# Performance work log

Measured on AMD Instinct MI355X. Metric: run time of the kernel, lower is better.

## Reference

```python
import jax, jax.numpy as jnp
import numpy as np

EM_STEPS = 2
C, N, H, F = 32, 200000, 4, 64


def setup_inputs() -> dict:
    key = jax.random.key(0)
    kq, kk, kv = jax.random.split(key, 3)
    Q = jax.random.normal(kq, (C, H, F), dtype=jnp.float32)
    K = jax.random.normal(kk, (N, H, F), dtype=jnp.float32)
    V = jax.random.normal(kv, (N, H, F), dtype=jnp.float32)
    return {"Q": Q, "K": K, "V": V}


def reference(Q, K, V):
    # EM-style recurrent cross-attention:
    #   scores[c,n,h] = sum_f centroid[c,h,f] * K[n,h,f] / sqrt(F)
    #   weights = softmax over clusters (axis 0)
    #   centroid[c,h,f] = sum_n weights[c,n,h] * V[n,h,f]
    scale = 1.0 / np.sqrt(np.float32(Q.shape[-1]))
    centroid = Q
    for _ in range(EM_STEPS):
        scores = jnp.einsum('chf,nhf->cnh', centroid, K) * scale  # (C,N,H)
        weights = jax.nn.softmax(scores, axis=0)                  # over clusters
        centroid = jnp.einsum('cnh,nhf->chf', weights, V)         # (C,H,F)
    return centroid
```

## Files before the change

### kernel.cpp

```cpp
#include <hip/hip_runtime.h>


#define CC 32
#define HH 4
#define FF 64
#define NB 64
#define WAVES 4
#define BLOCK 256
#define GX 192

__global__ __launch_bounds__(BLOCK, 3) void em_step_kernel(
    const float* __restrict__ cent_in,
    const float* __restrict__ Kp,
    const float* __restrict__ Vp,
    float* __restrict__ cent_out,
    int N)
{
    const int h    = blockIdx.y;
    const int tid  = threadIdx.x;
    const int wid  = tid >> 6;
    const int lane = tid & 63;

    __shared__ float cent[CC][FF];
    __shared__ float wlds[WAVES][NB][36];

    #pragma unroll
    for (int k = 0; k < (CC * FF) / BLOCK; ++k) {
        int i = k * BLOCK + tid;
        int c = i >> 6, f = i & 63;
        cent[c][f] = cent_in[(c * HH + h) * FF + f] * 0.125f;
    }
    __syncthreads();

    float acc[CC];
    #pragma unroll
    for (int c = 0; c < CC; ++c) acc[c] = 0.f;

    const int ngroups = (N + NB - 1) / NB;

    for (int g = blockIdx.x * WAVES + wid; g < ngroups; g += GX * WAVES) {
        const int n0 = g * NB;

        const int  n     = n0 + lane;
        const bool valid = (n < N);
        const int  ncl   = valid ? n : (N - 1);
        const float4* Kr = (const float4*)(Kp + ((size_t)ncl * HH + h) * FF);

        float s[CC];
        #pragma unroll
        for (int c = 0; c < CC; ++c) s[c] = 0.f;

        #pragma unroll 4
        for (int f4 = 0; f4 < FF / 4; ++f4) {
            float4 k4 = Kr[f4];
            #pragma unroll
            for (int c = 0; c < CC; ++c) {
                float4 ce = *(const float4*)&cent[c][f4 * 4];
                s[c] = fmaf(k4.x, ce.x, s[c]);
                s[c] = fmaf(k4.y, ce.y, s[c]);
                s[c] = fmaf(k4.z, ce.z, s[c]);
                s[c] = fmaf(k4.w, ce.w, s[c]);
            }
        }

        float m = s[0];
        #pragma unroll
        for (int c = 1; c < CC; ++c) m = fmaxf(m, s[c]);
        float sum = 0.f;
        #pragma unroll
        for (int c = 0; c < CC; ++c) { s[c] = __expf(s[c] - m); sum += s[c]; }
        float r = 1.0f / sum;
        if (!valid) r = 0.f;

        float4* wr = (float4*)&wlds[wid][lane][0];
        #pragma unroll
        for (int c4 = 0; c4 < 8; ++c4) {
            float4 w4;
            w4.x = s[c4 * 4 + 0] * r;
            w4.y = s[c4 * 4 + 1] * r;
            w4.z = s[c4 * 4 + 2] * r;
            w4.w = s[c4 * 4 + 3] * r;
            wr[c4] = w4;
        }

        #pragma unroll 4
        for (int j = 0; j < NB; ++j) {
            int nj  = n0 + j;
            int njc = nj < N ? nj : (N - 1);
            float v = Vp[((size_t)njc * HH + h) * FF + lane];
            #pragma unroll
            for (int c4 = 0; c4 < 8; ++c4) {
                float4 w4 = *(const float4*)&wlds[wid][j][c4 * 4];
                acc[c4 * 4 + 0] = fmaf(w4.x, v, acc[c4 * 4 + 0]);
                acc[c4 * 4 + 1] = fmaf(w4.y, v, acc[c4 * 4 + 1]);
                acc[c4 * 4 + 2] = fmaf(w4.z, v, acc[c4 * 4 + 2]);
                acc[c4 * 4 + 3] = fmaf(w4.w, v, acc[c4 * 4 + 3]);
            }
        }
    }

    __syncthreads();
    float* red = &wlds[0][0][0];
    #pragma unroll
    for (int c = 0; c < CC; ++c) red[(wid * CC + c) * FF + lane] = acc[c];
    __syncthreads();
    #pragma unroll
    for (int k = 0; k < (CC * FF) / BLOCK; ++k) {
        int o = k * BLOCK + tid;
        int c = o >> 6, f = o & 63;
        float val = red[(0 * CC + c) * FF + f]
                  + red[(1 * CC + c) * FF + f]
                  + red[(2 * CC + c) * FF + f]
                  + red[(3 * CC + c) * FF + f];
        atomicAdd(&cent_out[(c * HH + h) * FF + f], val);
    }
}

extern "C" void kernel_launch(void* const* d_in, const int* in_sizes, int n_in,
                              void* d_out, int out_size, void* d_ws, size_t ws_size,
                              hipStream_t stream)
{
    const float* Q = (const float*)d_in[0];
    const float* K = (const float*)d_in[1];
    const float* V = (const float*)d_in[2];
    float*       out   = (float*)d_out;
    float*       cent1 = (float*)d_ws;

    const int N = in_sizes[1] / (HH * FF);

    hipMemsetAsync(cent1, 0, CC * HH * FF * sizeof(float), stream);
    hipMemsetAsync(out,   0, CC * HH * FF * sizeof(float), stream);

    dim3 grid(GX, HH), block(BLOCK);
    em_step_kernel<<<grid, block, 0, stream>>>(Q,     K, V, cent1, N);
    em_step_kernel<<<grid, block, 0, stream>>>(cent1, K, V, out,   N);
}
```

Baseline: 894.7 us.

## Use packed FP32 FMA, transposed centroid LDS, and double-buffered V loads

Result: faster. 727.7 us (-18.7%).

```diff
diff --git a/kernel.cpp b/kernel.cpp
--- a/kernel.cpp
+++ b/kernel.cpp
@@ -5,11 +5,17 @@
 #define HH 4
 #define FF 64
 #define NB 64
-#define WAVES 4
-#define BLOCK 256
-#define GX 192
+#define WAVES 8
+#define BLOCK 512
+#define GX 128
 
-__global__ __launch_bounds__(BLOCK, 3) void em_step_kernel(
+typedef float f32x2 __attribute__((ext_vector_type(2)));
+
+__device__ __forceinline__ void pkfma(f32x2& d, f32x2 a, f32x2 b) {
+    asm("v_pk_fma_f32 %0, %1, %2, %0" : "+v"(d) : "v"(a), "v"(b));
+}
+
+__global__ __launch_bounds__(BLOCK, 4) void em_step_kernel(
     const float* __restrict__ cent_in,
     const float* __restrict__ Kp,
     const float* __restrict__ Vp,
@@ -21,20 +27,18 @@
     const int wid  = tid >> 6;
     const int lane = tid & 63;
 
-    __shared__ float cent[CC][FF];
+    __shared__ float centT[FF][CC];
     __shared__ float wlds[WAVES][NB][36];
 
-    #pragma unroll
-    for (int k = 0; k < (CC * FF) / BLOCK; ++k) {
-        int i = k * BLOCK + tid;
-        int c = i >> 6, f = i & 63;
-        cent[c][f] = cent_in[(c * HH + h) * FF + f] * 0.125f;
+    for (int i = tid; i < CC * FF; i += BLOCK) {
+        int c = i & (CC - 1), f = i >> 5;
+        centT[f][c] = cent_in[(c * HH + h) * FF + f] * 0.125f;
     }
     __syncthreads();
 
-    float acc[CC];
+    f32x2 acc2[16];
     #pragma unroll
-    for (int c = 0; c < CC; ++c) acc[c] = 0.f;
+    for (int p = 0; p < 16; ++p) acc2[p] = f32x2{0.f, 0.f};
 
     const int ngroups = (N + NB - 1) / NB;
 
@@ -46,29 +50,36 @@
         const int  ncl   = valid ? n : (N - 1);
         const float4* Kr = (const float4*)(Kp + ((size_t)ncl * HH + h) * FF);
 
-        float s[CC];
+        f32x2 s2[16];
         #pragma unroll
-        for (int c = 0; c < CC; ++c) s[c] = 0.f;
+        for (int p = 0; p < 16; ++p) s2[p] = f32x2{0.f, 0.f};
 
         #pragma unroll 4
         for (int f4 = 0; f4 < FF / 4; ++f4) {
             float4 k4 = Kr[f4];
+            float kv[4] = {k4.x, k4.y, k4.z, k4.w};
             #pragma unroll
-            for (int c = 0; c < CC; ++c) {
-                float4 ce = *(const float4*)&cent[c][f4 * 4];
-                s[c] = fmaf(k4.x, ce.x, s[c]);
-                s[c] = fmaf(k4.y, ce.y, s[c]);
-                s[c] = fmaf(k4.z, ce.z, s[c]);
-                s[c] = fmaf(k4.w, ce.w, s[c]);
+            for (int ff = 0; ff < 4; ++ff) {
+                f32x2 kk = {kv[ff], kv[ff]};
+                const float4* crow = (const float4*)&centT[f4 * 4 + ff][0];
+                #pragma unroll
+                for (int c8 = 0; c8 < 8; ++c8) {
+                    float4 ce = crow[c8];
+                    pkfma(s2[c8 * 2 + 0], kk, f32x2{ce.x, ce.y});
+                    pkfma(s2[c8 * 2 + 1], kk, f32x2{ce.z, ce.w});
+                }
             }
         }
 
-        float m = s[0];
+        float m = -3.0e38f;
         #pragma unroll
-        for (int c = 1; c < CC; ++c) m = fmaxf(m, s[c]);
+        for (int p = 0; p < 16; ++p) m = fmaxf(m, fmaxf(s2[p].x, s2[p].y));
         float sum = 0.f;
         #pragma unroll
-        for (int c = 0; c < CC; ++c) { s[c] = __expf(s[c] - m); sum += s[c]; }
+        for (int p = 0; p < 16; ++p) {
+            s2[p].x = __expf(s2[p].x - m); sum += s2[p].x;
+            s2[p].y = __expf(s2[p].y - m); sum += s2[p].y;
+        }
         float r = 1.0f / sum;
         if (!valid) r = 0.f;
 
@@ -76,42 +87,64 @@
         #pragma unroll
         for (int c4 = 0; c4 < 8; ++c4) {
             float4 w4;
-            w4.x = s[c4 * 4 + 0] * r;
-            w4.y = s[c4 * 4 + 1] * r;
-            w4.z = s[c4 * 4 + 2] * r;
-            w4.w = s[c4 * 4 + 3] * r;
+            w4.x = s2[2 * c4].x     * r;
+            w4.y = s2[2 * c4].y     * r;
+            w4.z = s2[2 * c4 + 1].x * r;
+            w4.w = s2[2 * c4 + 1].y * r;
             wr[c4] = w4;
         }
 
-        #pragma unroll 4
-        for (int j = 0; j < NB; ++j) {
-            int nj  = n0 + j;
-            int njc = nj < N ? nj : (N - 1);
-            float v = Vp[((size_t)njc * HH + h) * FF + lane];
+        const float* Vb = Vp + (size_t)h * FF + lane;
+
+        auto loadv = [&](float (&buf)[16], int jbase) {
             #pragma unroll
-            for (int c4 = 0; c4 < 8; ++c4) {
-                float4 w4 = *(const float4*)&wlds[wid][j][c4 * 4];
-                acc[c4 * 4 + 0] = fmaf(w4.x, v, acc[c4 * 4 + 0]);
-                acc[c4 * 4 + 1] = fmaf(w4.y, v, acc[c4 * 4 + 1]);
-                acc[c4 * 4 + 2] = fmaf(w4.z, v, acc[c4 * 4 + 2]);
-                acc[c4 * 4 + 3] = fmaf(w4.w, v, acc[c4 * 4 + 3]);
+            for (int jj = 0; jj < 16; ++jj) {
+                int nj  = n0 + jbase + jj;
+                int njc = nj < N ? nj : (N - 1);
+                buf[jj] = Vb[(size_t)njc * (HH * FF)];
             }
-        }
+        };
+        auto pv = [&](const float (&buf)[16], int jbase) {
+            #pragma unroll
+            for (int jj = 0; jj < 16; ++jj) {
+                int j = jbase + jj;
+                f32x2 vv = {buf[jj], buf[jj]};
+                const float4* wrow = (const float4*)&wlds[wid][j][0];
+                #pragma unroll
+                for (int c4 = 0; c4 < 8; ++c4) {
+                    float4 w4 = wrow[c4];
+                    pkfma(acc2[2 * c4 + 0], vv, f32x2{w4.x, w4.y});
+                    pkfma(acc2[2 * c4 + 1], vv, f32x2{w4.z, w4.w});
+                }
+            }
+        };
+
+        float va[16], vb[16];
+        loadv(va, 0);
+        loadv(vb, 16);
+        pv(va, 0);
+        loadv(va, 32);
+        pv(vb, 16);
+        loadv(vb, 48);
+        pv(va, 32);
+        pv(vb, 48);
     }
 
     __syncthreads();
     float* red = &wlds[0][0][0];
     #pragma unroll
-    for (int c = 0; c < CC; ++c) red[(wid * CC + c) * FF + lane] = acc[c];
+    for (int p = 0; p < 16; ++p) {
+        red[(wid * CC + 2 * p + 0) * FF + lane] = acc2[p].x;
+        red[(wid * CC + 2 * p + 1) * FF + lane] = acc2[p].y;
+    }
     __syncthreads();
     #pragma unroll
     for (int k = 0; k < (CC * FF) / BLOCK; ++k) {
         int o = k * BLOCK + tid;
         int c = o >> 6, f = o & 63;
-        float val = red[(0 * CC + c) * FF + f]
-                  + red[(1 * CC + c) * FF + f]
-                  + red[(2 * CC + c) * FF + f]
-                  + red[(3 * CC + c) * FF + f];
+        float val = 0.f;
+        #pragma unroll
+        for (int w = 0; w < WAVES; ++w) val += red[(w * CC + c) * FF + f];
         atomicAdd(&cent_out[(c * HH + h) * FF + f], val);
     }
 }
```
